# Optimization experiments

Measured on AMD Instinct MI355X. Metric: run time of the kernel, lower is better.

The kernel has to match this reference:

```python
import math
import jax, jax.numpy as jnp
import numpy as np

B, S, HID = 2, 2048, 2048
H, D = 32, 64  # num heads, head dim (H*D == HID)


def setup_inputs() -> dict:
    key = jax.random.key(0)
    ks = jax.random.split(key, 5)
    scale = 1.0 / math.sqrt(HID)
    return {
        "hidden_states": jax.random.normal(ks[0], (B, S, HID), dtype=jnp.float32),
        "attention_mask": jnp.zeros((B, S), dtype=jnp.float32),
        "wq": jax.random.normal(ks[1], (HID, HID), dtype=jnp.float32) * scale,
        "wk": jax.random.normal(ks[2], (HID, HID), dtype=jnp.float32) * scale,
        "wv": jax.random.normal(ks[3], (HID, HID), dtype=jnp.float32) * scale,
        "wo": jax.random.normal(ks[4], (HID, HID), dtype=jnp.float32) * scale,
    }


def reference(hidden_states, attention_mask, wq, wk, wv, wo):
    b, s, _ = hidden_states.shape
    # QKV projections (nn.Linear stores weight as [out, in]; y = x @ W^T)
    q = (hidden_states @ wq.T).reshape(b, s, H, D).transpose(0, 2, 1, 3)  # [B,H,S,D]
    k = (hidden_states @ wk.T).reshape(b, s, H, D).transpose(0, 2, 1, 3)
    v = (hidden_states @ wv.T).reshape(b, s, H, D).transpose(0, 2, 1, 3)
    # rotary_emb_ is None in the source module, so no RoPE is applied.
    scores = jnp.einsum("bhqd,bhkd->bhqk", q, k) / math.sqrt(D)  # [B,H,S,S]
    scores = scores + attention_mask.reshape(b, 1, 1, s)  # additive mask
    probs = jax.nn.softmax(scores, axis=-1)
    ctx = jnp.einsum("bhqk,bhkd->bhqd", probs, v)  # [B,H,S,D]
    ctx = ctx.transpose(0, 2, 1, 3).reshape(b, s, H * D)  # [B,S,HID]
    return ctx @ wo.T
```

## Files before the change

### kernel.cpp

```cpp
#include <hip/hip_runtime.h>

using bf16x8 = __attribute__((ext_vector_type(8))) __bf16;
using f32x4  = __attribute__((ext_vector_type(4))) float;
using uint2v = __attribute__((ext_vector_type(2))) unsigned int;

__device__ __forceinline__ unsigned short f2bf(float x) {
  unsigned int u = __float_as_uint(x);
  u += 0x7fffu + ((u >> 16) & 1u);
  return (unsigned short)(u >> 16);
}

__device__ __forceinline__ void gload16(const unsigned short* g, unsigned short* l) {
  __builtin_amdgcn_global_load_lds(
      (__attribute__((address_space(1))) void*)const_cast<unsigned short*>(g),
      (__attribute__((address_space(3))) void*)l, 16, 0, 0);
}

__global__ __launch_bounds__(256) void cvt_kernel(const float* __restrict__ in,
                                                  unsigned short* __restrict__ out) {
  const int i = blockIdx.x * 256 + threadIdx.x;
  const float4 v = ((const float4*)in)[i];
  ushort4 o;
  o.x = f2bf(v.x); o.y = f2bf(v.y); o.z = f2bf(v.z); o.w = f2bf(v.w);
  ((ushort4*)out)[i] = o;
}

template<int MODE>
__global__ __launch_bounds__(256)
void gemm_nt(const unsigned short* __restrict__ A,
             const unsigned short* __restrict__ Bw,
             float* __restrict__ Cf,
             unsigned short* __restrict__ Cq,
             int M, int N, int K)
{
  __shared__ unsigned short As[128 * 32];
  __shared__ unsigned short Bs[128 * 32];
  const int tid  = threadIdx.x;
  const int lane = tid & 63;
  const int wid  = tid >> 6;
  const int wr = wid >> 1, wc = wid & 1;
  const int lrow = lane & 15, lhi = lane >> 4;
  const int bn = blockIdx.x * 128;
  const int bm = blockIdx.y * 128;

  f32x4 acc[4][4] = {};

  const int srow = tid >> 2;
  const int scol = (tid & 3) * 8;
  const unsigned short* Ag0 = A  + (size_t)(bm + srow) * K + scol;
  const unsigned short* Ag1 = Ag0 + (size_t)64 * K;
  const unsigned short* Bg0 = Bw + (size_t)(bn + srow) * K + scol;
  const unsigned short* Bg1 = Bg0 + (size_t)64 * K;
  unsigned short* Ad0 = As + tid * 8;
  unsigned short* Ad1 = As + (256 + tid) * 8;
  unsigned short* Bd0 = Bs + tid * 8;
  unsigned short* Bd1 = Bs + (256 + tid) * 8;

  for (int k0 = 0; k0 < K; k0 += 32) {
    gload16(Ag0 + k0, Ad0);
    gload16(Ag1 + k0, Ad1);
    gload16(Bg0 + k0, Bd0);
    gload16(Bg1 + k0, Bd1);
    __syncthreads();
    bf16x8 af[4], bfr[4];
#pragma unroll
    for (int m = 0; m < 4; ++m)
      af[m] = *(const bf16x8*)(As + (wr * 64 + m * 16 + lrow) * 32 + lhi * 8);
#pragma unroll
    for (int n = 0; n < 4; ++n)
      bfr[n] = *(const bf16x8*)(Bs + (wc * 64 + n * 16 + lrow) * 32 + lhi * 8);
#pragma unroll
    for (int m = 0; m < 4; ++m)
#pragma unroll
      for (int n = 0; n < 4; ++n)
        acc[m][n] = __builtin_amdgcn_mfma_f32_16x16x32_bf16(af[m], bfr[n], acc[m][n], 0, 0, 0);
    __syncthreads();
  }

#pragma unroll
  for (int m = 0; m < 4; ++m) {
    const int row0 = bm + wr * 64 + m * 16 + lhi * 4;
#pragma unroll
    for (int n = 0; n < 4; ++n) {
      const int col = bn + wc * 64 + n * 16 + lrow;
#pragma unroll
      for (int r = 0; r < 4; ++r) {
        const int row = row0 + r;
        const float v = acc[m][n][r];
        if (MODE == 0) {
          const int which = col >> 11;
          const int h = (col >> 6) & 31;
          const int d = col & 63;
          const int b = row >> 11;
          const int s = row & 2047;
          if (which == 2) {
            Cq[(size_t)16777216 + ((size_t)(b * 32 + h) * 64 + d) * 2048 + s] = f2bf(v);
          } else {
            Cq[(((size_t)which * 64 + b * 32 + h) * 2048 + s) * 64 + d] = f2bf(v);
          }
        } else {
          Cf[(size_t)row * N + col] = v;
        }
      }
    }
  }
}

__global__ __launch_bounds__(256)
void attn_kernel(const unsigned short* __restrict__ QKV,
                 const float* __restrict__ mask,
                 unsigned short* __restrict__ Ctx)
{
  constexpr int S = 2048, D = 64, BH = 64;
  __shared__ unsigned short Klds[2][64 * 64];
  __shared__ unsigned short Vlds[2][64 * 64];
  __shared__ unsigned short PT[4][64 * 16];

  const int tid  = threadIdx.x;
  const int lane = tid & 63;
  const int wid  = tid >> 6;
  const int lrow = lane & 15;
  const int lhi  = lane >> 4;
  const int bh = blockIdx.y;
  const int b  = bh >> 5;
  const int h  = bh & 31;
  const int qbase = blockIdx.x * 64;

  const size_t qoff = (size_t)bh * S * D;
  const size_t koff = qoff + (size_t)BH * S * D;
  const size_t voff = koff + (size_t)BH * S * D;

  bf16x8 qa0, qa1;
  {
    const unsigned short* Qp = QKV + qoff + (size_t)(qbase + wid * 16 + lrow) * D + lhi * 8;
    qa0 = *(const bf16x8*)Qp;
    qa1 = *(const bf16x8*)(Qp + 32);
  }

  f32x4 oacc[4] = {};
  float srow[4] = {0.f, 0.f, 0.f, 0.f};

  const int strow  = tid >> 3;
  const int sswz   = ((tid & 7) ^ (strow & 7)) << 3;
  const unsigned short* Kg = QKV + koff + (size_t)strow * D + sswz;
  const unsigned short* Vg = QKV + voff + (size_t)strow * S + sswz;

  const float k1 = 0.125f * 1.44269504f;
  const unsigned ptbase =
      (unsigned)(uintptr_t)&PT[wid][0] + (unsigned)(lane * 8 + (lane >> 4) * 128);

  auto stage = [&](int t, int c) {
    const int kb = t * 64;
    gload16(Kg + (size_t)kb * D,          &Klds[c][0] + tid * 8);
    gload16(Kg + (size_t)kb * D + 32 * D, &Klds[c][0] + 2048 + tid * 8);
    gload16(Vg + kb,                      &Vlds[c][0] + tid * 8);
    gload16(Vg + kb + 32 * S,             &Vlds[c][0] + 2048 + tid * 8);
  };

  stage(0, 0);
  __syncthreads();

  for (int t = 0; t < S / 64; ++t) {
    const int kb  = t * 64;
    const int cur = t & 1;
    if (t + 1 < S / 64) stage(t + 1, cur ^ 1);

    float mkl[4];
#pragma unroll
    for (int f = 0; f < 4; ++f)
      mkl[f] = mask[(size_t)b * S + kb + lrow + 16 * f] * 1.44269504f;

    const unsigned short* Kc = &Klds[cur][0];
    f32x4 sacc[4] = {};
#pragma unroll
    for (int f = 0; f < 4; ++f) {
      const int krw = f * 16 + lrow;
      bf16x8 kf0 = *(const bf16x8*)(Kc + krw * 64 + ((lhi ^ (lrow & 7)) << 3));
      bf16x8 kf1 = *(const bf16x8*)(Kc + krw * 64 + (((lhi + 4) ^ (lrow & 7)) << 3));
      sacc[f] = __builtin_amdgcn_mfma_f32_16x16x32_bf16(qa0, kf0, sacc[f], 0, 0, 0);
      sacc[f] = __builtin_amdgcn_mfma_f32_16x16x32_bf16(qa1, kf1, sacc[f], 0, 0, 0);
    }

#pragma unroll
    for (int f = 0; f < 4; ++f)
#pragma unroll
      for (int r = 0; r < 4; ++r) {
        const float p = __builtin_amdgcn_exp2f(sacc[f][r] * k1 + mkl[f]);
        sacc[f][r] = p;
        srow[r] += p;
      }

    unsigned short* PTw = &PT[wid][0];
#pragma unroll
    for (int f = 0; f < 4; ++f) {
      unsigned w0, w1;
      asm("v_cvt_pk_bf16_f32 %0, %1, %2" : "=v"(w0) : "v"(sacc[f][0]), "v"(sacc[f][1]));
      asm("v_cvt_pk_bf16_f32 %0, %1, %2" : "=v"(w1) : "v"(sacc[f][2]), "v"(sacc[f][3]));
      uint2v w; w.x = w0; w.y = w1;
      *(uint2v*)(PTw + (lrow + 16 * f) * 16 + lhi * 4) = w;
    }

    const unsigned short* Vc = &Vlds[cur][0];
    uint2v r0, r1, r2, r3;
    asm volatile("ds_read_b64_tr_b16 %0, %1"             : "=v"(r0) : "v"(ptbase) : "memory");
    asm volatile("ds_read_b64_tr_b16 %0, %1 offset:128"  : "=v"(r1) : "v"(ptbase) : "memory");
    asm volatile("ds_read_b64_tr_b16 %0, %1 offset:1024" : "=v"(r2) : "v"(ptbase) : "memory");
    asm volatile("ds_read_b64_tr_b16 %0, %1 offset:1152" : "=v"(r3) : "v"(ptbase) : "memory");
    bf16x8 vb[2][4];
#pragma unroll
    for (int ks = 0; ks < 2; ++ks)
#pragma unroll
      for (int f = 0; f < 4; ++f) {
        const int dc = lrow + 16 * f;
        vb[ks][f] = *(const bf16x8*)(Vc + dc * 64 + (((ks * 4 + lhi) ^ (dc & 7)) << 3));
      }
    asm volatile("s_waitcnt lgkmcnt(0)" ::: "memory");
    __builtin_amdgcn_sched_barrier(0);
    union { struct { uint2v a, b; } u; bf16x8 v; } p0, p1;
    p0.u.a = r0; p0.u.b = r1;
    p1.u.a = r2; p1.u.b = r3;
#pragma unroll
    for (int f = 0; f < 4; ++f)
      oacc[f] = __builtin_amdgcn_mfma_f32_16x16x32_bf16(p0.v, vb[0][f], oacc[f], 0, 0, 0);
#pragma unroll
    for (int f = 0; f < 4; ++f)
      oacc[f] = __builtin_amdgcn_mfma_f32_16x16x32_bf16(p1.v, vb[1][f], oacc[f], 0, 0, 0);
    __syncthreads();
  }

#pragma unroll
  for (int off = 1; off < 16; off <<= 1)
#pragma unroll
    for (int r = 0; r < 4; ++r)
      srow[r] += __shfl_xor(srow[r], off, 64);

#pragma unroll
  for (int f = 0; f < 4; ++f) {
    const int d = lrow + 16 * f;
#pragma unroll
    for (int r = 0; r < 4; ++r) {
      const int q = qbase + wid * 16 + lhi * 4 + r;
      const float v = oacc[f][r] / srow[r];
      Ctx[((size_t)b * S + q) * 2048 + h * 64 + d] = f2bf(v);
    }
  }
}

extern "C" void kernel_launch(void* const* d_in, const int* in_sizes, int n_in,
                              void* d_out, int out_size, void* d_ws, size_t ws_size,
                              hipStream_t stream) {
  const float* X    = (const float*)d_in[0];
  const float* mask = (const float*)d_in[1];
  const float* wq   = (const float*)d_in[2];
  const float* wk   = (const float*)d_in[3];
  const float* wv   = (const float*)d_in[4];
  const float* wo   = (const float*)d_in[5];

  unsigned short* ws   = (unsigned short*)d_ws;
  unsigned short* Xb   = ws;
  unsigned short* Wcat = Xb + 8388608;
  unsigned short* Wob  = Wcat + 12582912;
  unsigned short* QKVb = Wob + 4194304;
  unsigned short* Ctxb = QKVb + 25165824;

  cvt_kernel<<<8192, 256, 0, stream>>>(X, Xb);
  cvt_kernel<<<4096, 256, 0, stream>>>(wq, Wcat);
  cvt_kernel<<<4096, 256, 0, stream>>>(wk, Wcat + 4194304);
  cvt_kernel<<<4096, 256, 0, stream>>>(wv, Wcat + 8388608);
  cvt_kernel<<<4096, 256, 0, stream>>>(wo, Wob);

  gemm_nt<0><<<dim3(48, 32), 256, 0, stream>>>(Xb, Wcat, nullptr, QKVb, 4096, 6144, 2048);

  attn_kernel<<<dim3(32, 64), 256, 0, stream>>>(QKVb, mask, Ctxb);

  gemm_nt<1><<<dim3(16, 32), 256, 0, stream>>>(Ctxb, Wob, (float*)d_out, nullptr, 4096, 2048, 2048);
}
```

Baseline: 498.4 us.

## Double-buffer GEMM with swizzled LDS, XCD-aware tiling, and MFMA-based softmax row sums

The GEMM gains double-buffered LDS staging with vmcnt-based waits, an XOR swizzle to cut LDS bank conflicts, a block-index remap that groups tiles per XCD, s_setprio around MFMA bursts, and launch bounds asking for 4 waves per SIMD. The attention kernel now computes the softmax denominator with extra MFMAs against a ones vector instead of per-lane adds plus cross-lane shuffles, and also sets priority around its MFMAs. These aim to overlap global loads with compute and cut VALU/LDS overhead, at the cost of more LDS per block and a few extra MFMAs per tile. The row sum now comes from bf16-rounded probabilities, which changes numerics slightly.

```diff
diff --git a/kernel.cpp b/kernel.cpp
--- a/kernel.cpp
+++ b/kernel.cpp
@@ -26,55 +26,77 @@
 }
 
 template<int MODE>
-__global__ __launch_bounds__(256)
-void gemm_nt(const unsigned short* __restrict__ A,
+__global__ __launch_bounds__(256, 4)
+void gemm128(const unsigned short* __restrict__ A,
              const unsigned short* __restrict__ Bw,
              float* __restrict__ Cf,
              unsigned short* __restrict__ Cq,
              int M, int N, int K)
 {
-  __shared__ unsigned short As[128 * 32];
-  __shared__ unsigned short Bs[128 * 32];
+  __shared__ unsigned short Sh[2][8192];
   const int tid  = threadIdx.x;
   const int lane = tid & 63;
   const int wid  = tid >> 6;
-  const int wr = wid >> 1, wc = wid & 1;
+  const int wr   = wid >> 1, wc = wid & 1;
   const int lrow = lane & 15, lhi = lane >> 4;
-  const int bn = blockIdx.x * 128;
-  const int bm = blockIdx.y * 128;
+
+  const int gY   = gridDim.y;
+  const int nwg  = gridDim.x * gY;
+  const int flat = blockIdx.x * gY + blockIdx.y;
+  const int swzb = (flat & 7) * (nwg >> 3) + (flat >> 3);
+  const int bn   = (swzb / gY) * 128;
+  const int bm   = (swzb % gY) * 128;
+  const int NT   = K >> 5;
+
+  const int srow = tid >> 2;
+  const int sswz = ((tid & 3) ^ ((tid >> 3) & 3)) << 3;
+  const unsigned short* AgS = A  + (size_t)(bm + srow) * K + sswz;
+  const unsigned short* BgS = Bw + (size_t)(bn + srow) * K + sswz;
+
+  const int coff = (lhi ^ ((lrow >> 1) & 3)) << 3;
+  int aoff[4], boff[4];
+#pragma unroll
+  for (int m = 0; m < 4; ++m) aoff[m] = (wr * 64 + m * 16 + lrow) * 32 + coff;
+#pragma unroll
+  for (int n = 0; n < 4; ++n) boff[n] = 4096 + (wc * 64 + n * 16 + lrow) * 32 + coff;
 
   f32x4 acc[4][4] = {};
 
-  const int srow = tid >> 2;
-  const int scol = (tid & 3) * 8;
-  const unsigned short* Ag0 = A  + (size_t)(bm + srow) * K + scol;
-  const unsigned short* Ag1 = Ag0 + (size_t)64 * K;
-  const unsigned short* Bg0 = Bw + (size_t)(bn + srow) * K + scol;
-  const unsigned short* Bg1 = Bg0 + (size_t)64 * K;
-  unsigned short* Ad0 = As + tid * 8;
-  unsigned short* Ad1 = As + (256 + tid) * 8;
-  unsigned short* Bd0 = Bs + tid * 8;
-  unsigned short* Bd1 = Bs + (256 + tid) * 8;
-
-  for (int k0 = 0; k0 < K; k0 += 32) {
-    gload16(Ag0 + k0, Ad0);
-    gload16(Ag1 + k0, Ad1);
-    gload16(Bg0 + k0, Bd0);
-    gload16(Bg1 + k0, Bd1);
-    __syncthreads();
+  auto stage = [&](int t, unsigned short* buf) {
+    const unsigned short* ag = AgS + (size_t)t * 32;
+    const unsigned short* bg = BgS + (size_t)t * 32;
+    gload16(ag,                  buf + tid * 8);
+    gload16(ag + (size_t)64 * K, buf + 2048 + tid * 8);
+    gload16(bg,                  buf + 4096 + tid * 8);
+    gload16(bg + (size_t)64 * K, buf + 6144 + tid * 8);
+  };
+
+  stage(0, &Sh[0][0]);
+
+  for (int t = 0; t < NT; ++t) {
+    if (t + 1 < NT) {
+      stage(t + 1, &Sh[(t + 1) & 1][0]);
+      asm volatile("s_waitcnt vmcnt(4)" ::: "memory");
+    } else {
+      asm volatile("s_waitcnt vmcnt(0)" ::: "memory");
+    }
+    __builtin_amdgcn_s_barrier();
+    asm volatile("" ::: "memory");
+
+    const unsigned short* cb = &Sh[t & 1][0];
     bf16x8 af[4], bfr[4];
 #pragma unroll
-    for (int m = 0; m < 4; ++m)
-      af[m] = *(const bf16x8*)(As + (wr * 64 + m * 16 + lrow) * 32 + lhi * 8);
-#pragma unroll
-    for (int n = 0; n < 4; ++n)
-      bfr[n] = *(const bf16x8*)(Bs + (wc * 64 + n * 16 + lrow) * 32 + lhi * 8);
+    for (int m = 0; m < 4; ++m) af[m]  = *(const bf16x8*)(cb + aoff[m]);
+#pragma unroll
+    for (int n = 0; n < 4; ++n) bfr[n] = *(const bf16x8*)(cb + boff[n]);
+    __builtin_amdgcn_s_setprio(1);
 #pragma unroll
     for (int m = 0; m < 4; ++m)
 #pragma unroll
       for (int n = 0; n < 4; ++n)
         acc[m][n] = __builtin_amdgcn_mfma_f32_16x16x32_bf16(af[m], bfr[n], acc[m][n], 0, 0, 0);
-    __syncthreads();
+    __builtin_amdgcn_s_setprio(0);
+    __builtin_amdgcn_s_barrier();
   }
 
 #pragma unroll
@@ -137,8 +159,12 @@
     qa1 = *(const bf16x8*)(Qp + 32);
   }
 
+  bf16x8 vones;
+#pragma unroll
+  for (int j = 0; j < 8; ++j) vones[j] = (__bf16)1.0f;
+
   f32x4 oacc[4] = {};
-  float srow[4] = {0.f, 0.f, 0.f, 0.f};
+  f32x4 osum = {};
 
   const int strow  = tid >> 3;
   const int sswz   = ((tid & 7) ^ (strow & 7)) << 3;
@@ -172,6 +198,7 @@
 
     const unsigned short* Kc = &Klds[cur][0];
     f32x4 sacc[4] = {};
+    __builtin_amdgcn_s_setprio(1);
 #pragma unroll
     for (int f = 0; f < 4; ++f) {
       const int krw = f * 16 + lrow;
@@ -180,15 +207,13 @@
       sacc[f] = __builtin_amdgcn_mfma_f32_16x16x32_bf16(qa0, kf0, sacc[f], 0, 0, 0);
       sacc[f] = __builtin_amdgcn_mfma_f32_16x16x32_bf16(qa1, kf1, sacc[f], 0, 0, 0);
     }
+    __builtin_amdgcn_s_setprio(0);
 
 #pragma unroll
     for (int f = 0; f < 4; ++f)
 #pragma unroll
-      for (int r = 0; r < 4; ++r) {
-        const float p = __builtin_amdgcn_exp2f(sacc[f][r] * k1 + mkl[f]);
-        sacc[f][r] = p;
-        srow[r] += p;
-      }
+      for (int r = 0; r < 4; ++r)
+        sacc[f][r] = __builtin_amdgcn_exp2f(sacc[f][r] * k1 + mkl[f]);
 
     unsigned short* PTw = &PT[wid][0];
 #pragma unroll
@@ -219,20 +244,18 @@
     union { struct { uint2v a, b; } u; bf16x8 v; } p0, p1;
     p0.u.a = r0; p0.u.b = r1;
     p1.u.a = r2; p1.u.b = r3;
+    __builtin_amdgcn_s_setprio(1);
 #pragma unroll
     for (int f = 0; f < 4; ++f)
       oacc[f] = __builtin_amdgcn_mfma_f32_16x16x32_bf16(p0.v, vb[0][f], oacc[f], 0, 0, 0);
+    osum = __builtin_amdgcn_mfma_f32_16x16x32_bf16(p0.v, vones, osum, 0, 0, 0);
 #pragma unroll
     for (int f = 0; f < 4; ++f)
       oacc[f] = __builtin_amdgcn_mfma_f32_16x16x32_bf16(p1.v, vb[1][f], oacc[f], 0, 0, 0);
+    osum = __builtin_amdgcn_mfma_f32_16x16x32_bf16(p1.v, vones, osum, 0, 0, 0);
+    __builtin_amdgcn_s_setprio(0);
     __syncthreads();
   }
-
-#pragma unroll
-  for (int off = 1; off < 16; off <<= 1)
-#pragma unroll
-    for (int r = 0; r < 4; ++r)
-      srow[r] += __shfl_xor(srow[r], off, 64);
 
 #pragma unroll
   for (int f = 0; f < 4; ++f) {
@@ -240,7 +263,7 @@
 #pragma unroll
     for (int r = 0; r < 4; ++r) {
       const int q = qbase + wid * 16 + lhi * 4 + r;
-      const float v = oacc[f][r] / srow[r];
+      const float v = oacc[f][r] / osum[r];
       Ctx[((size_t)b * S + q) * 2048 + h * 64 + d] = f2bf(v);
     }
   }
@@ -269,9 +292,9 @@
   cvt_kernel<<<4096, 256, 0, stream>>>(wv, Wcat + 8388608);
   cvt_kernel<<<4096, 256, 0, stream>>>(wo, Wob);
 
-  gemm_nt<0><<<dim3(48, 32), 256, 0, stream>>>(Xb, Wcat, nullptr, QKVb, 4096, 6144, 2048);
+  gemm128<0><<<dim3(48, 32), 256, 0, stream>>>(Xb, Wcat, nullptr, QKVb, 4096, 6144, 2048);
 
   attn_kernel<<<dim3(32, 64), 256, 0, stream>>>(QKVb, mask, Ctxb);
 
-  gemm_nt<1><<<dim3(16, 32), 256, 0, stream>>>(Ctxb, Wob, (float*)d_out, nullptr, 4096, 2048, 2048);
-}
+  gemm128<1><<<dim3(16, 32), 256, 0, stream>>>(Ctxb, Wob, (float*)d_out, nullptr, 4096, 2048, 2048);
+}
```

Result: faster. 458.9 us (-7.9%).
